# Kernel tuning notes

Measured on AMD Instinct MI355X. Metric: run time of the kernel, lower is better.

Reference implementation:

```python
import jax, jax.numpy as jnp
import numpy as np

N_NODES = 100000


def gcn_conv(x, W, b, src, dst, n_nodes):
    # PyG GCNConv: h = x @ W; add self-loops; symmetric normalization
    # out_i = sum_{j in N(i) U {i}} deg_i^{-1/2} deg_j^{-1/2} h_j + b
    h = x @ W                                   # [N, F_out]
    # append self-loops
    loop = jnp.arange(n_nodes, dtype=src.dtype)
    s = jnp.concatenate([src, loop])            # [E+N]
    d = jnp.concatenate([dst, loop])            # [E+N]
    deg = jax.ops.segment_sum(jnp.ones_like(d, dtype=h.dtype), d,
                              num_segments=n_nodes)   # [N]
    dinv = jnp.where(deg > 0, jax.lax.rsqrt(deg), 0.0)
    norm = dinv[s] * dinv[d]                    # [E+N]
    msg = h[s] * norm[:, None]                  # [E+N, F_out]
    out = jax.ops.segment_sum(msg, d, num_segments=n_nodes)
    return out + b


def setup_inputs() -> dict:
    key = jax.random.key(0)
    k1, k2, k3, k4 = jax.random.split(key, 4)
    input_dim, hidden_dim, num_classes = 128, 64, 40
    n_edges = 1600000
    x = jax.random.normal(k1, (N_NODES, input_dim), dtype=jnp.float32)
    edge_index = jax.random.randint(k2, (2, n_edges), 0, N_NODES, dtype=jnp.int64)
    # Glorot-style init for the two GCNConv layers
    W1 = jax.random.normal(k3, (input_dim, hidden_dim), dtype=jnp.float32) / np.sqrt(input_dim)
    b1 = jnp.zeros((hidden_dim,), dtype=jnp.float32)
    W2 = jax.random.normal(k4, (hidden_dim, num_classes), dtype=jnp.float32) / np.sqrt(hidden_dim)
    b2 = jnp.zeros((num_classes,), dtype=jnp.float32)
    return {"x": x, "edge_index": edge_index, "W1": W1, "b1": b1, "W2": W2, "b2": b2}


def reference(x, edge_index, W1, b1, W2, b2):
    src, dst = edge_index[0], edge_index[1]
    h = gcn_conv(x, W1, b1, src, dst, N_NODES)
    h = jax.nn.relu(h)
    out = gcn_conv(h, W2, b2, src, dst, N_NODES)
    return out
```

## Files before the change

### kernel.cpp

```cpp
#include <hip/hip_runtime.h>
#include <hip/hip_fp16.h>
#include <math.h>

#define NN 100000
#define NE 1600000
#define F0 128
#define F1 64
#define F2 40
#define NB 256
#define BSZ 391
#define CAP2 8192
#define CHUNK 3125
#define GEMM1_BLOCKS 1563
#define PART_BLOCKS 512

typedef _Float16 f16x8 __attribute__((ext_vector_type(8)));
typedef _Float16 f16x4 __attribute__((ext_vector_type(4)));
typedef float f32x4 __attribute__((ext_vector_type(4)));

__global__ __launch_bounds__(256) void k_init(const float* __restrict__ W1,
                                              const float* __restrict__ W2,
                                              _Float16* __restrict__ w1t,
                                              _Float16* __restrict__ w2t,
                                              int* __restrict__ bucketCnt) {
    int idx = blockIdx.x * 256 + threadIdx.x;
    if (idx <= NB) bucketCnt[idx] = 0;
    if (idx < 64 * 128) {
        int n = idx >> 7, k = idx & 127;
        w1t[idx] = (_Float16)W1[k * 64 + n];
    } else if (idx < 64 * 128 + 48 * 64) {
        int j = idx - 64 * 128;
        int n = j >> 6, k = j & 63;
        w2t[j] = (_Float16)(n < 40 ? W2[k * 40 + n] : 0.0f);
    }
}

__global__ __launch_bounds__(256) void k_g1p(const float* __restrict__ x,
                                             const _Float16* __restrict__ w1t,
                                             const int* __restrict__ src,
                                             const int* __restrict__ dst,
                                             int* __restrict__ bucketCnt,
                                             unsigned* __restrict__ bucket,
                                             _Float16* __restrict__ hs) {
    __shared__ _Float16 xl[64][136];
    __shared__ _Float16 wl[64][136];
    __shared__ int cnt[NB], base[NB];
    const int tid = threadIdx.x;

    if (blockIdx.x < GEMM1_BLOCKS) {
        const int row0 = blockIdx.x * 64;
        for (int i = tid; i < 1024; i += 256) {
            uint4 v = ((const uint4*)w1t)[i];
            *(uint4*)&wl[i >> 4][(i & 15) * 8] = v;
        }
        {
            int r = tid >> 2, part = tid & 3;
            int gr = row0 + r; if (gr >= NN) gr = NN - 1;
            const float* xr = x + (size_t)gr * F0 + part * 32;
            _Float16* dstp = &xl[r][part * 32];
            #pragma unroll
            for (int q = 0; q < 8; ++q) {
                float4 v = *(const float4*)&xr[q * 4];
                f16x4 h;
                h[0] = (_Float16)v.x; h[1] = (_Float16)v.y;
                h[2] = (_Float16)v.z; h[3] = (_Float16)v.w;
                *(f16x4*)&dstp[q * 4] = h;
            }
        }
        __syncthreads();

        const int wave = tid >> 6;
        const int lane = tid & 63;
        const int l16 = lane & 15;
        const int g8 = (lane >> 4) * 8;

        f32x4 acc[4] = {{0,0,0,0},{0,0,0,0},{0,0,0,0},{0,0,0,0}};
        #pragma unroll
        for (int k0 = 0; k0 < F0; k0 += 32) {
            f16x8 a = *(f16x8*)&xl[wave * 16 + l16][k0 + g8];
            #pragma unroll
            for (int ct = 0; ct < 4; ++ct) {
                f16x8 b = *(f16x8*)&wl[ct * 16 + l16][k0 + g8];
                acc[ct] = __builtin_amdgcn_mfma_f32_16x16x32_f16(a, b, acc[ct], 0, 0, 0);
            }
        }
        const int baserow = row0 + wave * 16 + (lane >> 4) * 4;
        #pragma unroll
        for (int j = 0; j < 4; ++j) {
            int gr = baserow + j;
            if (gr < NN) {
                #pragma unroll
                for (int ct = 0; ct < 4; ++ct)
                    hs[(size_t)gr * F1 + ct * 16 + l16] = (_Float16)acc[ct][j];
            }
        }
    } else {
        const int pb = blockIdx.x - GEMM1_BLOCKS;
        cnt[tid] = 0;
        __syncthreads();
        const int e0 = pb * CHUNK;
        const int e1 = e0 + CHUNK;
        for (int e = e0 + tid; e < e1; e += 256)
            atomicAdd(&cnt[dst[e] / BSZ], 1);
        __syncthreads();
        base[tid] = atomicAdd(&bucketCnt[tid], cnt[tid]);
        cnt[tid] = 0;
        __syncthreads();
        for (int e = e0 + tid; e < e1; e += 256) {
            int d = dst[e];
            int b = d / BSZ;
            int loc = d - b * BSZ;
            int ofs = atomicAdd(&cnt[b], 1);
            bucket[(size_t)b * CAP2 + base[b] + ofs] =
                ((unsigned)loc << 17) | (unsigned)src[e];
        }
    }
}

__global__ __launch_bounds__(512) void k_build(const int* __restrict__ bucketCnt,
                                               const unsigned* __restrict__ bucket,
                                               int* __restrict__ gCursor,
                                               int* __restrict__ rs,
                                               int* __restrict__ ce,
                                               int* __restrict__ csr,
                                               float* __restrict__ dinv) {
    __shared__ int cnt[512];
    __shared__ int sc[512];
    __shared__ int sh_base;

    const int tid = threadIdx.x;
    const int b = blockIdx.x;
    const int n0 = b * BSZ;
    const int nn = (NN - n0 < BSZ) ? (NN - n0) : BSZ;

    cnt[tid] = 0;
    __syncthreads();

    const int cntB = bucketCnt[b];
    const unsigned* bk = bucket + (size_t)b * CAP2;
    for (int idx = tid; idx < cntB; idx += 512)
        atomicAdd(&cnt[bk[idx] >> 17], 1);
    __syncthreads();

    sc[tid] = cnt[tid];
    __syncthreads();
    for (int off = 1; off < 512; off <<= 1) {
        int v = (tid >= off) ? sc[tid - off] : 0;
        __syncthreads();
        sc[tid] += v;
        __syncthreads();
    }

    const int T = sc[511];
    if (tid == 0) sh_base = atomicAdd(gCursor, T);
    __syncthreads();
    const int base = sh_base;

    if (tid < nn) {
        int c = cnt[tid];
        int excl = sc[tid] - c;
        rs[n0 + tid] = base + excl;
        ce[n0 + tid] = base + sc[tid];
        dinv[n0 + tid] = rsqrtf((float)(c + 1));
        sc[tid] = excl;
    }
    cnt[tid] = 0;
    __syncthreads();

    for (int idx = tid; idx < cntB; idx += 512) {
        unsigned p = bk[idx];
        int l = (int)(p >> 17);
        int ofs = atomicAdd(&cnt[l], 1);
        csr[base + sc[l] + ofs] = (int)(p & 0x1FFFFu);
    }
}

__device__ __forceinline__ void acc8s(float a[8], uint4 u, float s) {
    __half2 h0 = *(__half2*)&u.x, h1 = *(__half2*)&u.y;
    __half2 h2 = *(__half2*)&u.z, h3 = *(__half2*)&u.w;
    float2 f0 = __half22float2(h0), f1 = __half22float2(h1);
    float2 f2 = __half22float2(h2), f3 = __half22float2(h3);
    a[0] = fmaf(s, f0.x, a[0]); a[1] = fmaf(s, f0.y, a[1]);
    a[2] = fmaf(s, f1.x, a[2]); a[3] = fmaf(s, f1.y, a[3]);
    a[4] = fmaf(s, f2.x, a[4]); a[5] = fmaf(s, f2.y, a[5]);
    a[6] = fmaf(s, f3.x, a[6]); a[7] = fmaf(s, f3.y, a[7]);
}

__device__ __forceinline__ void acc4(float a[4], uint2 u) {
    __half2 h0 = *(__half2*)&u.x, h1 = *(__half2*)&u.y;
    float2 f0 = __half22float2(h0), f1 = __half22float2(h1);
    a[0] += f0.x; a[1] += f0.y; a[2] += f1.x; a[3] += f1.y;
}

__global__ __launch_bounds__(512) void k_fuse(const int* __restrict__ rs,
                                              const int* __restrict__ ce,
                                              const int* __restrict__ csr,
                                              const _Float16* __restrict__ hs,
                                              const float* __restrict__ dinv,
                                              const float* __restrict__ b1,
                                              const _Float16* __restrict__ w2t,
                                              _Float16* __restrict__ hs2) {
    __shared__ _Float16 al[64][72];
    __shared__ _Float16 wl2[48][72];
    const int tid = threadIdx.x;
    const int row0 = blockIdx.x * 64;

    if (tid < 384)
        *(uint4*)&wl2[tid >> 3][(tid & 7) * 8] = ((const uint4*)w2t)[tid];

    {
        int r = tid >> 3, g = tid & 7;
        int i = row0 + r; if (i >= NN) i = NN - 1;
        const __half* hsh = (const __half*)hs;
        float dvi = dinv[i];
        float acc[8] = {0, 0, 0, 0, 0, 0, 0, 0};
        acc8s(acc, *(const uint4*)&hsh[(size_t)i * F1 + g * 8], dvi);
        int k = rs[i], end = ce[i];
        for (; k + 4 <= end; k += 4) {
            int s0 = csr[k], s1 = csr[k + 1], s2 = csr[k + 2], s3 = csr[k + 3];
            float d0 = dinv[s0], d1 = dinv[s1], d2 = dinv[s2], d3 = dinv[s3];
            uint4 u0 = *(const uint4*)&hsh[(size_t)s0 * F1 + g * 8];
            uint4 u1 = *(const uint4*)&hsh[(size_t)s1 * F1 + g * 8];
            uint4 u2 = *(const uint4*)&hsh[(size_t)s2 * F1 + g * 8];
            uint4 u3 = *(const uint4*)&hsh[(size_t)s3 * F1 + g * 8];
            acc8s(acc, u0, d0); acc8s(acc, u1, d1);
            acc8s(acc, u2, d2); acc8s(acc, u3, d3);
        }
        for (; k < end; ++k) {
            int s0 = csr[k];
            acc8s(acc, *(const uint4*)&hsh[(size_t)s0 * F1 + g * 8], dinv[s0]);
        }
        float4 c0 = *(const float4*)&b1[g * 8];
        float4 c1 = *(const float4*)&b1[g * 8 + 4];
        f16x8 o;
        o[0] = (_Float16)fmaxf(fmaf(dvi, acc[0], c0.x), 0.0f);
        o[1] = (_Float16)fmaxf(fmaf(dvi, acc[1], c0.y), 0.0f);
        o[2] = (_Float16)fmaxf(fmaf(dvi, acc[2], c0.z), 0.0f);
        o[3] = (_Float16)fmaxf(fmaf(dvi, acc[3], c0.w), 0.0f);
        o[4] = (_Float16)fmaxf(fmaf(dvi, acc[4], c1.x), 0.0f);
        o[5] = (_Float16)fmaxf(fmaf(dvi, acc[5], c1.y), 0.0f);
        o[6] = (_Float16)fmaxf(fmaf(dvi, acc[6], c1.z), 0.0f);
        o[7] = (_Float16)fmaxf(fmaf(dvi, acc[7], c1.w), 0.0f);
        *(f16x8*)&al[r][g * 8] = o;
    }
    __syncthreads();

    const int wave = tid >> 6;
    const int lane = tid & 63;
    const int l16 = lane & 15;
    const int g8 = (lane >> 4) * 8;

    for (int t = wave; t < 12; t += 8) {
        int rt = t / 3, ct = t - rt * 3;
        f32x4 acc = {0, 0, 0, 0};
        #pragma unroll
        for (int k0 = 0; k0 < F1; k0 += 32) {
            f16x8 a = *(f16x8*)&al[rt * 16 + l16][k0 + g8];
            f16x8 b = *(f16x8*)&wl2[ct * 16 + l16][k0 + g8];
            acc = __builtin_amdgcn_mfma_f32_16x16x32_f16(a, b, acc, 0, 0, 0);
        }
        int col = ct * 16 + l16;
        int baserow = row0 + rt * 16 + (lane >> 4) * 4;
        if (col < F2) {
            #pragma unroll
            for (int j = 0; j < 4; ++j) {
                int gr = baserow + j;
                if (gr < NN)
                    hs2[(size_t)gr * F2 + col] = (_Float16)(acc[j] * dinv[gr]);
            }
        }
    }
}

__global__ __launch_bounds__(320) void k_gather2(const int* __restrict__ rs,
                                                 const int* __restrict__ ce,
                                                 const int* __restrict__ csr,
                                                 const __half* __restrict__ hs2,
                                                 const float* __restrict__ dinv,
                                                 const float* __restrict__ b,
                                                 float* __restrict__ outp) {
    int t = blockIdx.x * 320 + threadIdx.x;
    int i = t / 10;
    int g = t - i * 10;
    float acc[4] = {0, 0, 0, 0};
    acc4(acc, *(const uint2*)&hs2[(size_t)i * F2 + g * 4]);
    int k = rs[i], end = ce[i];
    for (; k + 4 <= end; k += 4) {
        int s0 = csr[k], s1 = csr[k + 1], s2 = csr[k + 2], s3 = csr[k + 3];
        uint2 u0 = *(const uint2*)&hs2[(size_t)s0 * F2 + g * 4];
        uint2 u1 = *(const uint2*)&hs2[(size_t)s1 * F2 + g * 4];
        uint2 u2 = *(const uint2*)&hs2[(size_t)s2 * F2 + g * 4];
        uint2 u3 = *(const uint2*)&hs2[(size_t)s3 * F2 + g * 4];
        acc4(acc, u0); acc4(acc, u1); acc4(acc, u2); acc4(acc, u3);
    }
    for (; k < end; ++k)
        acc4(acc, *(const uint2*)&hs2[(size_t)csr[k] * F2 + g * 4]);

    float dv = dinv[i];
    float4 bb = *(const float4*)&b[g * 4];
    float4 r;
    r.x = fmaf(dv, acc[0], bb.x);
    r.y = fmaf(dv, acc[1], bb.y);
    r.z = fmaf(dv, acc[2], bb.z);
    r.w = fmaf(dv, acc[3], bb.w);
    *(float4*)&outp[(size_t)i * F2 + g * 4] = r;
}

extern "C" void kernel_launch(void* const* d_in, const int* in_sizes, int n_in,
                              void* d_out, int out_size, void* d_ws, size_t ws_size,
                              hipStream_t stream) {
    const float* x  = (const float*)d_in[0];
    const int*   ei = (const int*)d_in[1];
    const float* W1 = (const float*)d_in[2];
    const float* b1 = (const float*)d_in[3];
    const float* W2 = (const float*)d_in[4];
    const float* b2 = (const float*)d_in[5];
    float* out = (float*)d_out;

    const int* src = ei;
    const int* dst = ei + NE;

    float*    dinv      = (float*)d_ws;
    int*      rs        = (int*)d_ws + 102400;
    int*      ce        = (int*)d_ws + 204800;
    int*      bucketCnt = (int*)d_ws + 307200;
    _Float16* w1t       = (_Float16*)((int*)d_ws + 308224);
    _Float16* w2t       = (_Float16*)((int*)d_ws + 312320);
    int*      csr       = (int*)d_ws + 313856;
    _Float16* hs        = (_Float16*)((int*)d_ws + 313856 + NE);
    unsigned* bucket    = (unsigned*)((int*)d_ws + 313856 + NE + 3200000);
    _Float16* hs2       = (_Float16*)bucket;

    k_init<<<44, 256, 0, stream>>>(W1, W2, w1t, w2t, bucketCnt);
    k_g1p<<<GEMM1_BLOCKS + PART_BLOCKS, 256, 0, stream>>>(x, w1t, src, dst,
                                                          bucketCnt, bucket, hs);
    k_build<<<NB, 512, 0, stream>>>(bucketCnt, bucket, bucketCnt + NB,
                                    rs, ce, csr, dinv);
    k_fuse<<<GEMM1_BLOCKS, 512, 0, stream>>>(rs, ce, csr, hs, dinv, b1, w2t, hs2);
    k_gather2<<<NN / 32, 320, 0, stream>>>(rs, ce, csr, (const __half*)hs2,
                                           dinv, b2, out);
}
```

Baseline: 131.3 us.

## Interleave partition blocks with GEMM blocks and stream x directly into MFMA fragments

```diff
diff --git a/kernel.cpp b/kernel.cpp
--- a/kernel.cpp
+++ b/kernel.cpp
@@ -42,60 +42,63 @@
                                              int* __restrict__ bucketCnt,
                                              unsigned* __restrict__ bucket,
                                              _Float16* __restrict__ hs) {
-    __shared__ _Float16 xl[64][136];
     __shared__ _Float16 wl[64][136];
+    __shared__ _Float16 st[64][72];
     __shared__ int cnt[NB], base[NB];
     const int tid = threadIdx.x;
-
-    if (blockIdx.x < GEMM1_BLOCKS) {
-        const int row0 = blockIdx.x * 64;
-        for (int i = tid; i < 1024; i += 256) {
-            uint4 v = ((const uint4*)w1t)[i];
-            *(uint4*)&wl[i >> 4][(i & 15) * 8] = v;
-        }
-        {
-            int r = tid >> 2, part = tid & 3;
-            int gr = row0 + r; if (gr >= NN) gr = NN - 1;
-            const float* xr = x + (size_t)gr * F0 + part * 32;
-            _Float16* dstp = &xl[r][part * 32];
-            #pragma unroll
-            for (int q = 0; q < 8; ++q) {
-                float4 v = *(const float4*)&xr[q * 4];
-                f16x4 h;
-                h[0] = (_Float16)v.x; h[1] = (_Float16)v.y;
-                h[2] = (_Float16)v.z; h[3] = (_Float16)v.w;
-                *(f16x4*)&dstp[q * 4] = h;
-            }
-        }
+    const int b = blockIdx.x;
+
+    bool isPart = (b < 2048) && ((b & 3) == 3);
+    if (!isPart) {
+        const int gb = (b < 2048) ? (b - ((b + 1) >> 2)) : (b - PART_BLOCKS);
+        const int row0 = gb * 64;
+        for (int i = tid; i < 1024; i += 256)
+            *(uint4*)&wl[i >> 4][(i & 15) * 8] = ((const uint4*)w1t)[i];
         __syncthreads();
 
         const int wave = tid >> 6;
         const int lane = tid & 63;
         const int l16 = lane & 15;
-        const int g8 = (lane >> 4) * 8;
+        const int hi = lane >> 4;
+        const int g8 = hi * 8;
+
+        int gra = row0 + wave * 16 + l16; if (gra >= NN) gra = NN - 1;
+        const float* xr = x + (size_t)gra * F0;
 
         f32x4 acc[4] = {{0,0,0,0},{0,0,0,0},{0,0,0,0},{0,0,0,0}};
         #pragma unroll
         for (int k0 = 0; k0 < F0; k0 += 32) {
-            f16x8 a = *(f16x8*)&xl[wave * 16 + l16][k0 + g8];
+            float4 v0 = *(const float4*)&xr[k0 + g8];
+            float4 v1 = *(const float4*)&xr[k0 + g8 + 4];
+            f16x8 a;
+            a[0] = (_Float16)v0.x; a[1] = (_Float16)v0.y;
+            a[2] = (_Float16)v0.z; a[3] = (_Float16)v0.w;
+            a[4] = (_Float16)v1.x; a[5] = (_Float16)v1.y;
+            a[6] = (_Float16)v1.z; a[7] = (_Float16)v1.w;
             #pragma unroll
             for (int ct = 0; ct < 4; ++ct) {
-                f16x8 b = *(f16x8*)&wl[ct * 16 + l16][k0 + g8];
-                acc[ct] = __builtin_amdgcn_mfma_f32_16x16x32_f16(a, b, acc[ct], 0, 0, 0);
+                f16x8 bb = *(f16x8*)&wl[ct * 16 + l16][k0 + g8];
+                acc[ct] = __builtin_amdgcn_mfma_f32_16x16x32_f16(a, bb, acc[ct], 0, 0, 0);
             }
         }
-        const int baserow = row0 + wave * 16 + (lane >> 4) * 4;
+
         #pragma unroll
-        for (int j = 0; j < 4; ++j) {
-            int gr = baserow + j;
-            if (gr < NN) {
-                #pragma unroll
-                for (int ct = 0; ct < 4; ++ct)
-                    hs[(size_t)gr * F1 + ct * 16 + l16] = (_Float16)acc[ct][j];
-            }
+        for (int ct = 0; ct < 4; ++ct)
+            #pragma unroll
+            for (int j = 0; j < 4; ++j)
+                st[wave * 16 + hi * 4 + j][ct * 16 + l16] = (_Float16)acc[ct][j];
+
+        int rr = lane >> 2;
+        int cc = lane & 3;
+        int grow = row0 + wave * 16 + rr;
+        if (grow < NN) {
+            uint4 w0 = *(uint4*)&st[wave * 16 + rr][cc * 16];
+            uint4 w1 = *(uint4*)&st[wave * 16 + rr][cc * 16 + 8];
+            *(uint4*)&hs[(size_t)grow * F1 + cc * 16] = w0;
+            *(uint4*)&hs[(size_t)grow * F1 + cc * 16 + 8] = w1;
         }
     } else {
-        const int pb = blockIdx.x - GEMM1_BLOCKS;
+        const int pb = b >> 2;
         cnt[tid] = 0;
         __syncthreads();
         const int e0 = pb * CHUNK;
@@ -108,10 +111,10 @@
         __syncthreads();
         for (int e = e0 + tid; e < e1; e += 256) {
             int d = dst[e];
-            int b = d / BSZ;
-            int loc = d - b * BSZ;
-            int ofs = atomicAdd(&cnt[b], 1);
-            bucket[(size_t)b * CAP2 + base[b] + ofs] =
+            int bk = d / BSZ;
+            int loc = d - bk * BSZ;
+            int ofs = atomicAdd(&cnt[bk], 1);
+            bucket[(size_t)bk * CAP2 + base[bk] + ofs] =
                 ((unsigned)loc << 17) | (unsigned)src[e];
         }
     }
```

After: 148.2 us. +12.9%, slower.
